# Performance work log

Measured on AMD Instinct MI355X. Metric: run time of the kernel, lower is better.

Reference implementation:

```python
import jax, jax.numpy as jnp
import numpy as np

HID = 50  # hardcoded hidden size in the module


def setup_inputs() -> dict:
    key = jax.random.key(0)
    ks = jax.random.split(key, 7)
    B, T, F = 32, 2048, 1024
    s = 1.0 / np.sqrt(HID)  # pytorch LSTM/Linear init bound
    sl = 1.0 / np.sqrt(HID)
    return {
        "input": jax.random.normal(ks[0], (B, T, F), jnp.float32),
        "W_ih": jax.random.uniform(ks[1], (4 * HID, F), jnp.float32, -s, s),
        "W_hh": jax.random.uniform(ks[2], (4 * HID, HID), jnp.float32, -s, s),
        "b_ih": jax.random.uniform(ks[3], (4 * HID,), jnp.float32, -s, s),
        "b_hh": jax.random.uniform(ks[4], (4 * HID,), jnp.float32, -s, s),
        "W_lin": jax.random.uniform(ks[5], (F, HID), jnp.float32, -sl, sl),
        "b_lin": jax.random.uniform(ks[6], (F,), jnp.float32, -sl, sl),
    }


def reference(input, W_ih, W_hh, b_ih, b_hh, W_lin, b_lin):
    # The torch code never passes (h_t, c_t) back into nn.LSTM, so every
    # timestep runs a single LSTM cell with ZERO initial hidden/cell state.
    # With h_prev = 0 the W_hh contribution vanishes; gates depend on x only.
    # PyTorch gate order: i, f, g, o.
    gates = jnp.einsum('btf,gf->btg', input, W_ih) + b_ih + b_hh  # [B,T,4H]
    i, f, g, o = jnp.split(gates, 4, axis=-1)
    c = jax.nn.sigmoid(i) * jnp.tanh(g)          # c_prev = 0 => f-gate term drops
    h = jax.nn.sigmoid(o) * jnp.tanh(c)          # [B,T,H]
    out = jnp.einsum('bth,fh->btf', h, W_lin) + b_lin  # [B,T,F]
    return out
```

## Files before the change

### kernel.cpp

```cpp
#include <hip/hip_runtime.h>


typedef _Float16 f16;
typedef f16 f16x8 __attribute__((ext_vector_type(8)));
typedef float f32x4 __attribute__((ext_vector_type(4)));

#define W1S_ELEMS (32 * 10 * 64)
#define W2S_ELEMS (64 * 2 * 64)

__device__ f16x8 g_w1s[W1S_ELEMS];
__device__ f16x8 g_w2s[W2S_ELEMS];
__device__ float g_bias[160];

__device__ __forceinline__ int pack_map(int j) {
    return (j < 50) ? j : (j < 150) ? (j + 50) : -1;
}

__global__ __launch_bounds__(256) void prep_kernel(
    const float* __restrict__ W_ih, const float* __restrict__ b_ih,
    const float* __restrict__ b_hh, const float* __restrict__ W_lin)
{
    int idx = blockIdx.x * 256 + threadIdx.x;
    if (idx < W1S_ELEMS) {
        int lane = idx & 63, rest = idx >> 6;
        int gt = rest % 10, ks = rest / 10;
        int prow = gt * 16 + (lane & 15);
        int oj = pack_map(prow);
        int k0 = ks * 32 + ((lane >> 4) << 3);
        f16x8 v;
        #pragma unroll
        for (int j = 0; j < 8; ++j)
            v[j] = (f16)((oj >= 0) ? W_ih[oj * 1024 + k0 + j] : 0.f);
        g_w1s[idx] = v;
    } else if (idx < W1S_ELEMS + W2S_ELEMS) {
        int i2 = idx - W1S_ELEMS;
        int lane = i2 & 63, rest = i2 >> 6;
        int ks = rest & 1, ct = rest >> 1;
        int ocol = ct * 16 + (lane & 15);
        int k0 = ks * 32 + ((lane >> 4) << 3);
        f16x8 v;
        #pragma unroll
        for (int j = 0; j < 8; ++j) {
            int k = k0 + j;
            v[j] = (f16)((k < 50) ? W_lin[ocol * 50 + k] : 0.f);
        }
        g_w2s[i2] = v;
    } else if (idx < W1S_ELEMS + W2S_ELEMS + 160) {
        int i3 = idx - (W1S_ELEMS + W2S_ELEMS);
        int oj = pack_map(i3);
        g_bias[i3] = (oj >= 0) ? (b_ih[oj] + b_hh[oj]) : 0.f;
    }
}

__device__ __forceinline__ int gaddr(int row, int col) {
    int c = col + ((row & 15) << 2);
    if (c >= 160) c -= 160;
    return row * 160 + c;
}

__device__ __forceinline__ float fast_tanh(float v) {
    float t = __expf(-2.f * v);
    return (1.f - t) / (1.f + t);
}

#define GLOAD16(gp, lp) __builtin_amdgcn_global_load_lds( \
    (const __attribute__((address_space(1))) void*)(gp),  \
    (__attribute__((address_space(3))) void*)(lp), 16, 0, 0)

__global__ __launch_bounds__(256, 4) void lstm_fused(
    const float* __restrict__ x, const float* __restrict__ blin,
    float* __restrict__ out)
{
    __shared__ __align__(16) char smem[40960];
    float* gs = (float*)smem;
    f16*   hs = (f16*)smem;

    const int tid  = threadIdx.x;
    const int lane = tid & 63;
    const int wv   = tid >> 6;
    const int lcol = lane & 15;
    const int l4   = lane >> 4;
    const long row0 = (long)blockIdx.x * 64;
    const int wrow = wv * 16;

    const int bid   = blockIdx.x;
    const int koff  = (bid * 5 + (bid >> 8) * 8) & 31;
    const int ctoff = ((bid * 11 + (bid >> 8) * 16) & 63) + wv * 16;

    const int wt0 = (wv < 2) ? wv * 3 : 6 + (wv - 2) * 2;
    const int nw  = (wv < 2) ? 3 : 2;

    const int sw = ((lane & 7) ^ (lane >> 3)) << 2;
    const float* xsrc0 = x + (row0 + (2 * wv) * 8 + (lane >> 3)) * 1024 + sw;
    const float* xsrc1 = x + (row0 + (2 * wv + 1) * 8 + (lane >> 3)) * 1024 + sw;

    char* xs0 = smem + (2 * wv) * 1024;
    char* xs1 = smem + (2 * wv + 1) * 1024;

    #define STAGE(c, par) do {                                                 \
        const int c_ = (c);                                                    \
        const int p_ = (par);                                                  \
        GLOAD16(xsrc0 + c_ * 32, xs0 + p_ * 8192);                             \
        GLOAD16(xsrc1 + c_ * 32, xs1 + p_ * 8192);                             \
        _Pragma("unroll")                                                      \
        for (int wti = 0; wti < 3; ++wti)                                      \
            if (wti < nw)                                                      \
                GLOAD16((const f16x8*)g_w1s + c_ * 640 + (wt0 + wti) * 64 + lane, \
                        smem + 16384 + p_ * 10240 + (wt0 + wti) * 1024);       \
    } while (0)

    f32x4 acc[10];
    #pragma unroll
    for (int g = 0; g < 10; ++g) acc[g] = (f32x4){0.f, 0.f, 0.f, 0.f};

    STAGE(koff, 0);
    STAGE((koff + 1) & 31, 1);

    const int abyte = (wrow + lcol) * 128;
    const int au0 = ((2 * l4 + 0) ^ (lcol & 7)) << 4;
    const int au1 = ((2 * l4 + 1) ^ (lcol & 7)) << 4;

    for (int t = 0; t < 32; ++t) {
        if (t == 31)       asm volatile("s_waitcnt vmcnt(0)" ::: "memory");
        else if (wv < 2)   asm volatile("s_waitcnt vmcnt(5)" ::: "memory");
        else               asm volatile("s_waitcnt vmcnt(4)" ::: "memory");
        __builtin_amdgcn_sched_barrier(0);
        __builtin_amdgcn_s_barrier();

        const int par = t & 1;
        const char* ab = smem + par * 8192 + abyte;
        float4 qa = *(const float4*)(ab + au0);
        float4 qb = *(const float4*)(ab + au1);
        f16x8 af = { (f16)qa.x, (f16)qa.y, (f16)qa.z, (f16)qa.w,
                     (f16)qb.x, (f16)qb.y, (f16)qb.z, (f16)qb.w };
        const f16x8* wb = (const f16x8*)(smem + 16384 + par * 10240) + lane;
        #pragma unroll
        for (int g = 0; g < 10; ++g) {
            f16x8 bf = wb[g * 64];
            acc[g] = __builtin_amdgcn_mfma_f32_16x16x32_f16(af, bf, acc[g], 0, 0, 0);
        }

        asm volatile("s_waitcnt lgkmcnt(0)" ::: "memory");
        __builtin_amdgcn_sched_barrier(0);
        __builtin_amdgcn_s_barrier();
        if (t < 30) STAGE((t + 2 + koff) & 31, par);
    }

    #pragma unroll
    for (int g = 0; g < 10; ++g) {
        float bb = g_bias[g * 16 + lcol];
        #pragma unroll
        for (int r = 0; r < 4; ++r)
            gs[gaddr(wrow + l4 * 4 + r, g * 16 + lcol)] = acc[g][r] + bb;
    }
    __syncthreads();

    const int nrow = tid >> 2, sub = tid & 3;
    const int c0 = sub * 13;
    float hreg[13];
    #pragma unroll
    for (int j = 0; j < 13; ++j) {
        int c = c0 + j;
        float hv = 0.f;
        if (c < 50) {
            float iv = gs[gaddr(nrow, c)];
            float gv = gs[gaddr(nrow, 50 + c)];
            float ov = gs[gaddr(nrow, 100 + c)];
            float cv = fast_tanh(gv) / (1.f + __expf(-iv));
            hv = fast_tanh(cv) / (1.f + __expf(-ov));
        }
        hreg[j] = hv;
    }
    __syncthreads();

    #pragma unroll
    for (int j = 0; j < 13; ++j)
        hs[nrow * 72 + c0 + j] = (f16)hreg[j];
    if (sub == 3) {
        #pragma unroll
        for (int c = 52; c < 64; ++c) hs[nrow * 72 + c] = (f16)0.f;
    }
    __syncthreads();

    const int hrow = wrow + lcol;
    f16x8 bh0 = *(const f16x8*)(hs + hrow * 72 + l4 * 8);
    f16x8 bh1 = *(const f16x8*)(hs + hrow * 72 + 32 + l4 * 8);
    float* orow = out + (row0 + hrow) * 1024;

    #pragma unroll 4
    for (int t2 = 0; t2 < 64; ++t2) {
        int ct = (t2 + ctoff) & 63;
        float4 bl = *(const float4*)(blin + ct * 16 + l4 * 4);
        f32x4 o = { bl.x, bl.y, bl.z, bl.w };
        const f16x8* w2b = g_w2s + ct * 128 + lane;
        o = __builtin_amdgcn_mfma_f32_16x16x32_f16(w2b[0],  bh0, o, 0, 0, 0);
        o = __builtin_amdgcn_mfma_f32_16x16x32_f16(w2b[64], bh1, o, 0, 0, 0);
        __builtin_nontemporal_store(o, (f32x4*)(orow + ct * 16 + l4 * 4));
    }
}

extern "C" void kernel_launch(void* const* d_in, const int* in_sizes, int n_in,
                              void* d_out, int out_size, void* d_ws, size_t ws_size,
                              hipStream_t stream) {
    const float* x     = (const float*)d_in[0];
    const float* W_ih  = (const float*)d_in[1];
    const float* b_ih  = (const float*)d_in[3];
    const float* b_hh  = (const float*)d_in[4];
    const float* W_lin = (const float*)d_in[5];
    const float* b_lin = (const float*)d_in[6];
    float* out = (float*)d_out;

    int prep_total = W1S_ELEMS + W2S_ELEMS + 160;
    prep_kernel<<<(prep_total + 255) / 256, 256, 0, stream>>>(
        W_ih, b_ih, b_hh, W_lin);

    lstm_fused<<<1024, 256, 0, stream>>>(x, b_lin, out);
}
```

Before: 130.7 us.

## Stage output tiles through LDS for fully coalesced row-contiguous stores

The second GEMM now has each wave compute column tiles for 16 rows at a time and write the results into a swizzled LDS buffer. The whole block then writes contiguous 2KB row segments to global memory with nontemporal stores, replacing scattered 64-byte per-lane stores. The goal is fully coalesced output writes on a store-bound kernel, at the cost of extra LDS traffic and barriers. It also switches the second tanh to the library tanhf, which is likely slower but more accurate.

New measurement: 161.1 us. +23.3%, slower.

```diff
diff --git a/kernel.cpp b/kernel.cpp
--- a/kernel.cpp
+++ b/kernel.cpp
@@ -74,6 +74,7 @@
     __shared__ __align__(16) char smem[40960];
     float* gs = (float*)smem;
     f16*   hs = (f16*)smem;
+    float* ls = (float*)smem;
 
     const int tid  = threadIdx.x;
     const int lane = tid & 63;
@@ -85,7 +86,6 @@
 
     const int bid   = blockIdx.x;
     const int koff  = (bid * 5 + (bid >> 8) * 8) & 31;
-    const int ctoff = ((bid * 11 + (bid >> 8) * 16) & 63) + wv * 16;
 
     const int wt0 = (wv < 2) ? wv * 3 : 6 + (wv - 2) * 2;
     const int nw  = (wv < 2) ? 3 : 2;
@@ -167,7 +167,7 @@
             float gv = gs[gaddr(nrow, 50 + c)];
             float ov = gs[gaddr(nrow, 100 + c)];
             float cv = fast_tanh(gv) / (1.f + __expf(-iv));
-            hv = fast_tanh(cv) / (1.f + __expf(-ov));
+            hv = tanhf(cv) / (1.f + __expf(-ov));
         }
         hreg[j] = hv;
     }
@@ -182,20 +182,41 @@
     }
     __syncthreads();
 
-    const int hrow = wrow + lcol;
-    f16x8 bh0 = *(const f16x8*)(hs + hrow * 72 + l4 * 8);
-    f16x8 bh1 = *(const f16x8*)(hs + hrow * 72 + 32 + l4 * 8);
-    float* orow = out + (row0 + hrow) * 1024;
-
-    #pragma unroll 4
-    for (int t2 = 0; t2 < 64; ++t2) {
-        int ct = (t2 + ctoff) & 63;
-        float4 bl = *(const float4*)(blin + ct * 16 + l4 * 4);
-        f32x4 o = { bl.x, bl.y, bl.z, bl.w };
-        const f16x8* w2b = g_w2s + ct * 128 + lane;
-        o = __builtin_amdgcn_mfma_f32_16x16x32_f16(w2b[0],  bh0, o, 0, 0, 0);
-        o = __builtin_amdgcn_mfma_f32_16x16x32_f16(w2b[64], bh1, o, 0, 0, 0);
-        __builtin_nontemporal_store(o, (f32x4*)(orow + ct * 16 + l4 * 4));
+    f16x8 bh[4][2];
+    #pragma unroll
+    for (int g = 0; g < 4; ++g) {
+        bh[g][0] = *(const f16x8*)(hs + (g * 16 + lcol) * 72 + l4 * 8);
+        bh[g][1] = *(const f16x8*)(hs + (g * 16 + lcol) * 72 + 32 + l4 * 8);
+    }
+    __syncthreads();
+
+    #pragma unroll
+    for (int g = 0; g < 4; ++g) {
+        #pragma unroll
+        for (int half = 0; half < 2; ++half) {
+            #pragma unroll
+            for (int i = 0; i < 8; ++i) {
+                int ctl = wv * 8 + i;
+                int ct  = half * 32 + ctl;
+                float4 bl = *(const float4*)(blin + ct * 16 + l4 * 4);
+                f32x4 o = { bl.x, bl.y, bl.z, bl.w };
+                const f16x8* w2b = g_w2s + ct * 128 + lane;
+                o = __builtin_amdgcn_mfma_f32_16x16x32_f16(w2b[0],  bh[g][0], o, 0, 0, 0);
+                o = __builtin_amdgcn_mfma_f32_16x16x32_f16(w2b[64], bh[g][1], o, 0, 0, 0);
+                int u = ctl * 4 + l4;
+                *(f32x4*)(ls + lcol * 512 + ((u ^ (lcol & 7)) << 2)) = o;
+            }
+            __syncthreads();
+            #pragma unroll
+            for (int it = 0; it < 8; ++it) {
+                int row = it * 2 + (tid >> 7);
+                int u = tid & 127;
+                f32x4 v = *(const f32x4*)(ls + row * 512 + ((u ^ (row & 7)) << 2));
+                __builtin_nontemporal_store(v,
+                    (f32x4*)(out + (row0 + g * 16 + row) * 1024 + half * 512 + u * 4));
+            }
+            __syncthreads();
+        }
     }
 }
 
```
